# Optimization experiments

Hardware: AMD Instinct MI355X
Metric: run time of the kernel (lower is better)

## Reference

```python
import jax, jax.numpy as jnp
import numpy as np

DIM = 1024
NUM_HEADS = 16
BATCH = 4
SEQ = 2048
SCALE = (DIM // NUM_HEADS) ** -0.5
MASK_VAL = -10000000.0


def setup_inputs() -> dict:
    key = jax.random.key(0)
    k1, k2, k3, k4 = jax.random.split(key, 4)
    inputs = jax.random.normal(k1, (BATCH, SEQ, DIM), dtype=jnp.float32)
    # xavier-ish scaling for weights
    W_qkv = jax.random.normal(k2, (3 * DIM, DIM), dtype=jnp.float32) * (1.0 / np.sqrt(DIM))
    W_fc = jax.random.normal(k3, (DIM, DIM), dtype=jnp.float32) * (1.0 / np.sqrt(DIM))
    b_fc = jnp.zeros((DIM,), dtype=jnp.float32)
    padding_mask = jax.random.randint(k4, (BATCH, SEQ), 0, 2, dtype=jnp.int32)
    return {"inputs": inputs, "W_qkv": W_qkv, "W_fc": W_fc, "b_fc": b_fc,
            "padding_mask": padding_mask}


def reference(inputs, W_qkv, W_fc, b_fc, padding_mask):
    B, N, C = inputs.shape
    H = NUM_HEADS
    Dh = C // H
    # qkv projection (torch Linear: x @ W.T), [B,N,3C]
    qkv = jnp.einsum('bnc,oc->bno', inputs, W_qkv)
    qkv = qkv.reshape(B, N, 3, H, Dh).transpose(2, 0, 3, 1, 4)  # [3,B,H,N,Dh]
    q, k, v = qkv[0], qkv[1], qkv[2]
    att = jnp.einsum('bhqd,bhkd->bhqk', q, k) * SCALE  # [B,H,N,N]
    mask = padding_mask[:, None, None, :]              # [B,1,1,N]
    att = jnp.where(mask > 0, jnp.float32(MASK_VAL), att)
    att = jax.nn.softmax(att, axis=-1)
    x = jnp.einsum('bhqk,bhkd->bhqd', att, v)          # [B,H,N,Dh]
    x = x.transpose(0, 2, 1, 3).reshape(B, N, C)       # [B,N,C]
    out = jnp.einsum('bnc,oc->bno', x, W_fc) + b_fc
    return out
```

## Files before the change

kernel.cpp:

```cpp
#include <hip/hip_runtime.h>
#include <stdint.h>

constexpr int kDim  = 1024;
constexpr int kH    = 16;
constexpr int kB    = 4;
constexpr int kSeq  = 2048;
constexpr int kDh   = 64;
constexpr int kMTot = kB * kSeq;
constexpr int kNQkv = 3 * kDim;
constexpr float kScale = 0.125f;
constexpr float kLog2e = 1.44269504088896f;
constexpr float kC1    = kScale * kLog2e;
constexpr float kMaxSub = 10.0f;
constexpr float kMk2Un   = -kMaxSub * kLog2e;
constexpr float kMk2Mask = -1.0e9f;
constexpr int kPld = 72;
constexpr int kCld = 136;

typedef __attribute__((ext_vector_type(8))) short short8;
typedef __attribute__((ext_vector_type(4))) float floatx4;

__device__ __forceinline__ unsigned short f2bf(float f) {
  union { float f; unsigned u; } v; v.f = f;
  unsigned r = v.u + 0x7fffu + ((v.u >> 16) & 1u);
  return (unsigned short)(r >> 16);
}
__device__ __forceinline__ unsigned short f2bf_fast(float f) {
  union { float f; unsigned u; } v; v.f = f;
  return (unsigned short)((v.u + 0x8000u) >> 16);
}
__device__ __forceinline__ float vexp2(float x) {
  float r; asm("v_exp_f32 %0, %1" : "=v"(r) : "v"(x)); return r;
}
__device__ __forceinline__ void gl2lds16(const void* g, void* l) {
  __builtin_amdgcn_global_load_lds(
      (const __attribute__((address_space(1))) unsigned int*)g,
      (__attribute__((address_space(3))) unsigned int*)l, 16, 0, 0);
}

__global__ void __launch_bounds__(256) cvt_scan(
    const float4* __restrict__ x, const float4* __restrict__ wq,
    const float4* __restrict__ wf,
    ushort4* __restrict__ xb, ushort4* __restrict__ wqb, ushort4* __restrict__ wfb,
    const int* __restrict__ pm, int* __restrict__ cidx, int* __restrict__ nkd) {
  const int X4  = (kMTot * kDim) / 4;
  const int WQ4 = (kNQkv * kDim) / 4;
  const int NCVT = 12288;
  if (blockIdx.x >= NCVT) {
    const int b = blockIdx.x - NCVT;
    const int t = threadIdx.x;
    const int lane = t & 63, wv = t >> 6;
    __shared__ int wsum[4];
    __shared__ int woff[5];
    int base = t * 8;
    int keep[8]; int cnt = 0;
#pragma unroll
    for (int j = 0; j < 8; j++) {
      keep[j] = (pm[b * kSeq + base + j] <= 0) ? 1 : 0;
      cnt += keep[j];
    }
    int pre = cnt;
#pragma unroll
    for (int off = 1; off < 64; off <<= 1) {
      int v = __shfl_up(pre, off, 64);
      if (lane >= off) pre += v;
    }
    int excl = pre - cnt;
    if (lane == 63) wsum[wv] = pre;
    __syncthreads();
    if (t == 0) {
      int s = 0;
#pragma unroll
      for (int w = 0; w < 4; w++) { woff[w] = s; s += wsum[w]; }
      woff[4] = s;
      nkd[b] = s;
    }
    __syncthreads();
    const int nk = woff[4];
    int kp = woff[wv] + excl;
#pragma unroll
    for (int j = 0; j < 8; j++) {
      int n = base + j;
      int pos = keep[j] ? kp : nk + (n - kp);
      cidx[b * kSeq + pos] = b * kSeq + n;
      kp += keep[j];
    }
    return;
  }
  int i = blockIdx.x * 256 + threadIdx.x;
  float4 v; ushort4* dst;
  if (i < X4)            { v = x[i];             dst = xb  + i; }
  else if (i < X4 + WQ4) { v = wq[i - X4];       dst = wqb + (i - X4); }
  else                   { v = wf[i - X4 - WQ4]; dst = wfb + (i - X4 - WQ4); }
  ushort4 o;
  o.x = f2bf(v.x); o.y = f2bf(v.y); o.z = f2bf(v.z); o.w = f2bf(v.w);
  *dst = o;
}

__global__ void __launch_bounds__(512, 2) gemm_qkv(
    const unsigned short* __restrict__ xb, const unsigned short* __restrict__ wqb,
    const int* __restrict__ cidx, const int* __restrict__ nkd,
    unsigned short* __restrict__ qb, unsigned short* __restrict__ kb,
    unsigned short* __restrict__ vtb) {
  const int tN = blockIdx.x * 256, tM = blockIdx.y * 256;
  const int which = tN >> 10;
  const int b = tM >> 11, tMloc = tM & 2047;
  if (which != 0) {
    if (tMloc >= nkd[b]) return;
  }
  extern __shared__ __attribute__((aligned(16))) unsigned short smem[];
  unsigned short* As0 = smem;
  unsigned short* Bs0 = smem + 16384;
  unsigned short* As1 = smem + 32768;
  unsigned short* Bs1 = smem + 49152;

  const int t = threadIdx.x;
  const int lane = t & 63, wv = t >> 6;
  const int wm = (wv >> 2) << 7;
  const int wn = (wv & 3) << 6;
  const int lrow = lane & 15, quad = lane >> 4, l7 = lane & 7;
  const int srow = t >> 3;
  const int pu8 = (t & 7) * 8;
  const int lu8 = ((t & 7) ^ (srow & 7)) * 8;
  const int off0 = (quad ^ l7) * 8;

  const unsigned short* arow[4];
#pragma unroll
  for (int p = 0; p < 4; p++) {
    int r = tM + srow + p * 64;
    int rid = (which == 0) ? r : cidx[r];
    arow[p] = xb + (int64_t)rid * kDim + lu8;
  }
  const unsigned short* brow = wqb + (int64_t)(tN + srow) * kDim + lu8;

  floatx4 acc[8][4];
  floatx4 zero = {0.f, 0.f, 0.f, 0.f};
#pragma unroll
  for (int mi = 0; mi < 8; mi++)
#pragma unroll
    for (int ni = 0; ni < 4; ni++) acc[mi][ni] = zero;

#define STAGE_B(buf, p, k0) gl2lds16(brow + (int64_t)(p) * 64 * kDim + (k0), \
                                     (buf) + ((p) * 64 + srow) * 64 + pu8)
#define STAGE_A(buf, p, k0) gl2lds16(arow[p] + (k0), \
                                     (buf) + ((p) * 64 + srow) * 64 + pu8)
#define BARRIER() { asm volatile("" ::: "memory"); \
                    __builtin_amdgcn_s_barrier(); \
                    asm volatile("" ::: "memory"); }
#define LDA(q) { \
    const unsigned short* Ar0_ = Ac + (wm + (2*(q)) * 16 + lrow) * 64; \
    const unsigned short* Ar1_ = Ac + (wm + (2*(q)+1) * 16 + lrow) * 64; \
    af00 = *(const short8*)(Ar0_ + off0); \
    af01 = *(const short8*)(Ar0_ + (off0 ^ 32)); \
    af10 = *(const short8*)(Ar1_ + off0); \
    af11 = *(const short8*)(Ar1_ + (off0 ^ 32)); }
#define MFMAQ(q) { \
    __builtin_amdgcn_s_setprio(1); \
    _Pragma("unroll") \
    for (int ni = 0; ni < 4; ni++) { \
      acc[2*(q)][ni]   = __builtin_amdgcn_mfma_f32_16x16x32_bf16(af00, bfr[ni][0], acc[2*(q)][ni],   0, 0, 0); \
      acc[2*(q)+1][ni] = __builtin_amdgcn_mfma_f32_16x16x32_bf16(af10, bfr[ni][0], acc[2*(q)+1][ni], 0, 0, 0); \
    } \
    _Pragma("unroll") \
    for (int ni = 0; ni < 4; ni++) { \
      acc[2*(q)][ni]   = __builtin_amdgcn_mfma_f32_16x16x32_bf16(af01, bfr[ni][1], acc[2*(q)][ni],   0, 0, 0); \
      acc[2*(q)+1][ni] = __builtin_amdgcn_mfma_f32_16x16x32_bf16(af11, bfr[ni][1], acc[2*(q)+1][ni], 0, 0, 0); \
    } \
    __builtin_amdgcn_s_setprio(0); }

  STAGE_B(Bs0, 0, 0); STAGE_B(Bs0, 1, 0); STAGE_B(Bs0, 2, 0); STAGE_B(Bs0, 3, 0);
  STAGE_A(As0, 0, 0); STAGE_A(As0, 2, 0); STAGE_A(As0, 1, 0); STAGE_A(As0, 3, 0);
  asm volatile("s_waitcnt vmcnt(2)" ::: "memory");
  BARRIER();

  for (int tt = 0; tt < 16; ++tt) {
    unsigned short* Ac = (tt & 1) ? As1 : As0;
    unsigned short* Bc = (tt & 1) ? Bs1 : Bs0;
    unsigned short* An = (tt & 1) ? As0 : As1;
    unsigned short* Bn = (tt & 1) ? Bs0 : Bs1;
    const int kn = (tt + 1) * 64;
    const bool more = (tt < 15);

    short8 bfr[4][2];
    short8 af00, af01, af10, af11;

#pragma unroll
    for (int ni = 0; ni < 4; ni++) {
      const unsigned short* Br_ = Bc + (wn + ni * 16 + lrow) * 64;
      bfr[ni][0] = *(const short8*)(Br_ + off0);
      bfr[ni][1] = *(const short8*)(Br_ + (off0 ^ 32));
    }
    LDA(0);
    if (more) { STAGE_B(Bn, 0, kn); STAGE_B(Bn, 1, kn); }
    BARRIER();
    MFMAQ(0);
    BARRIER();
    LDA(1);
    if (more) { STAGE_B(Bn, 2, kn); STAGE_B(Bn, 3, kn); }
    BARRIER();
    MFMAQ(1);
    if (more) { asm volatile("s_waitcnt vmcnt(4)" ::: "memory"); }
    else      { asm volatile("s_waitcnt vmcnt(0)" ::: "memory"); }
    BARRIER();
    LDA(2);
    if (more) { STAGE_A(An, 0, kn); STAGE_A(An, 2, kn); }
    BARRIER();
    MFMAQ(2);
    BARRIER();
    LDA(3);
    if (more) { STAGE_A(An, 1, kn); STAGE_A(An, 3, kn); }
    BARRIER();
    MFMAQ(3);
    asm volatile("s_waitcnt vmcnt(2)" ::: "memory");
    BARRIER();
  }
#undef STAGE_B
#undef STAGE_A
#undef LDA
#undef MFMAQ

  unsigned short* Cs = smem;
  const bool vblk = (which == 2);
  const int h4 = (tN >> 6) & 15;
#pragma unroll
  for (int h = 0; h < 2; h++) {
    const bool writer = (((wv & 3) >> 1) == h);
    const int cwn = (wv & 1) * 64;
    if (!vblk) {
      if (writer) {
#pragma unroll
        for (int mi = 0; mi < 8; mi++)
#pragma unroll
          for (int ni = 0; ni < 4; ni++)
#pragma unroll
            for (int r = 0; r < 4; r++) {
              int row = wm + mi * 16 + quad * 4 + r;
              int c = cwn + ni * 16 + lrow;
              Cs[row * kCld + c] = f2bf(acc[mi][ni][r]);
            }
      }
      asm volatile("s_waitcnt lgkmcnt(0)" ::: "memory");
      BARRIER();
      unsigned short* qk = (which == 0) ? qb : kb;
#pragma unroll
      for (int g = 0; g < 2; g++) {
        int hh = (h4 + h * 2 + g) & 15;
        unsigned short* base = qk + ((int64_t)((b << 4) + hh) << 17)
                               + (int64_t)tMloc * 64;
#pragma unroll
        for (int it = 0; it < 4; it++) {
          int off = it * 4096 + t * 8;
          int n = off >> 6;
          int d = off & 63;
          *(short8*)(base + off) = *(const short8*)(Cs + n * kCld + g * 64 + d);
        }
      }
      BARRIER();
    } else {
      if (writer) {
#pragma unroll
        for (int mi = 0; mi < 8; mi++)
#pragma unroll
          for (int ni = 0; ni < 4; ni++)
#pragma unroll
            for (int r = 0; r < 4; r++) {
              int row = wm + mi * 16 + quad * 4 + r;
              int c = cwn + ni * 16 + lrow;
              Cs[c * 264 + row] = f2bf(acc[mi][ni][r]);
            }
      }
      asm volatile("s_waitcnt lgkmcnt(0)" ::: "memory");
      BARRIER();
#pragma unroll
      for (int g = 0; g < 2; g++) {
        int hh = (h4 + h * 2 + g) & 15;
        unsigned short* vbase = vtb + ((int64_t)((b << 4) + hh) << 17) + tMloc;
#pragma unroll
        for (int it = 0; it < 4; it++) {
          int off = it * 512 + t;
          int d = off >> 5, c8 = off & 31;
          *(short8*)(vbase + (int64_t)d * 2048 + c8 * 8) =
              *(const short8*)(Cs + (g * 64 + d) * 264 + c8 * 8);
        }
      }
      BARRIER();
    }
  }
#undef BARRIER
}

__global__ void __launch_bounds__(256, 4) attn(
    const unsigned short* __restrict__ qb, const unsigned short* __restrict__ kb,
    const unsigned short* __restrict__ vtb, const int* __restrict__ nkd,
    unsigned short* __restrict__ xab) {
  __shared__ __attribute__((aligned(16))) unsigned short Ks[64 * 64];
  __shared__ __attribute__((aligned(16))) unsigned short Vs[64 * 64];
  __shared__ __attribute__((aligned(16))) unsigned short Ps[4][2][16 * kPld];

  const int t = threadIdx.x, lane = t & 63, wv = t >> 6;
  const int lrow = lane & 15, quad = lane >> 4, l7 = lane & 7;
  const int qblk = blockIdx.x & 15, bh = blockIdx.x >> 4;
  const int b = bh >> 4, h = bh & 15;
  const int q0 = qblk * 128;
  const int srow = t >> 3;
  const int pu8 = (t & 7) * 8;
  const int lu8 = ((t & 7) ^ (srow & 7)) * 8;
  const int off0 = (quad ^ l7) * 8;

  const int nk  = nkd[b];
  const int nkt = (nk + 63) >> 6;

  const unsigned short* Qb0 = qb + ((int64_t)bh * kSeq + q0 + wv * 16 + lrow) * kDh;
  short8 qf[2][2];
  qf[0][0] = *(const short8*)(Qb0 + quad * 8);
  qf[0][1] = *(const short8*)(Qb0 + 32 + quad * 8);
  qf[1][0] = *(const short8*)(Qb0 + 64 * kDh + quad * 8);
  qf[1][1] = *(const short8*)(Qb0 + 64 * kDh + 32 + quad * 8);

  float l_run[2][4];
  floatx4 o_acc[2][4];
  floatx4 zero = {0.f, 0.f, 0.f, 0.f};
#pragma unroll
  for (int t2 = 0; t2 < 2; t2++) {
#pragma unroll
    for (int r = 0; r < 4; r++) l_run[t2][r] = 0.f;
#pragma unroll
    for (int di = 0; di < 4; di++) o_acc[t2][di] = zero;
  }

  const unsigned short* Kbase = kb  + (int64_t)bh * kSeq * kDh;
  const unsigned short* Vbase = vtb + (int64_t)bh * kDh * kSeq;

  for (int kt = 0; kt < nkt; ++kt) {
    const int k0 = kt * 64;
    {
      int r0 = srow, r1 = srow + 32;
      gl2lds16(Kbase + (int64_t)(k0 + r0) * kDh + lu8, Ks + r0 * 64 + pu8);
      gl2lds16(Kbase + (int64_t)(k0 + r1) * kDh + lu8, Ks + r1 * 64 + pu8);
      gl2lds16(Vbase + (int64_t)r0 * kSeq + k0 + lu8,  Vs + r0 * 64 + pu8);
      gl2lds16(Vbase + (int64_t)r1 * kSeq + k0 + lu8,  Vs + r1 * 64 + pu8);
    }
    __syncthreads();

    floatx4 s[2][4];
#pragma unroll
    for (int ni = 0; ni < 4; ni++) {
      const unsigned short* Kr = Ks + (ni * 16 + lrow) * 64;
      short8 kf0 = *(const short8*)(Kr + off0);
      short8 kf1 = *(const short8*)(Kr + (off0 ^ 32));
#pragma unroll
      for (int t2 = 0; t2 < 2; t2++) {
        floatx4 tmp = __builtin_amdgcn_mfma_f32_16x16x32_bf16(qf[t2][0], kf0, zero, 0, 0, 0);
        s[t2][ni]   = __builtin_amdgcn_mfma_f32_16x16x32_bf16(qf[t2][1], kf1, tmp, 0, 0, 0);
      }
    }
    float mk2[4];
#pragma unroll
    for (int c = 0; c < 4; c++)
      mk2[c] = (k0 + c * 16 + lrow < nk) ? kMk2Un : kMk2Mask;

#pragma unroll
    for (int t2 = 0; t2 < 2; t2++) {
      unsigned short* Pw = &Ps[wv][t2][0];
#pragma unroll
      for (int r = 0; r < 4; r++) {
        int prow = (quad * 4 + r) * kPld + lrow;
#pragma unroll
        for (int c = 0; c < 4; c++) {
          float p = vexp2(fmaf(s[t2][c][r], kC1, mk2[c]));
          l_run[t2][r] += p;
          Pw[prow + c * 16] = f2bf_fast(p);
        }
      }
    }
    asm volatile("s_waitcnt lgkmcnt(0)" ::: "memory");

#pragma unroll
    for (int ks = 0; ks < 2; ks++) {
      short8 pf0 = *(const short8*)(&Ps[wv][0][0] + lrow * kPld + ks * 32 + quad * 8);
      short8 pf1 = *(const short8*)(&Ps[wv][1][0] + lrow * kPld + ks * 32 + quad * 8);
      const int voff = off0 ^ (ks * 32);
#pragma unroll
      for (int di = 0; di < 4; di++) {
        short8 vf = *(const short8*)(Vs + (di * 16 + lrow) * 64 + voff);
        o_acc[0][di] = __builtin_amdgcn_mfma_f32_16x16x32_bf16(pf0, vf, o_acc[0][di], 0, 0, 0);
        o_acc[1][di] = __builtin_amdgcn_mfma_f32_16x16x32_bf16(pf1, vf, o_acc[1][di], 0, 0, 0);
      }
    }
    __syncthreads();
  }

#pragma unroll
  for (int t2 = 0; t2 < 2; t2++) {
#pragma unroll
    for (int r = 0; r < 4; r++) {
      float l = l_run[t2][r];
      l += __shfl_xor(l, 1, 64);
      l += __shfl_xor(l, 2, 64);
      l += __shfl_xor(l, 4, 64);
      l += __shfl_xor(l, 8, 64);
      float inv = 1.0f / l;
      int n = q0 + t2 * 64 + wv * 16 + quad * 4 + r;
      int64_t rowbase = ((int64_t)b * kSeq + n) * kDim + h * kDh;
#pragma unroll
      for (int di = 0; di < 4; di++)
        xab[rowbase + di * 16 + lrow] = f2bf(o_acc[t2][di][r] * inv);
    }
  }
}

__global__ void __launch_bounds__(256) gemm_fc(
    const unsigned short* __restrict__ xab, const unsigned short* __restrict__ wfb,
    const float* __restrict__ bfc, float* __restrict__ out) {
  __shared__ __attribute__((aligned(16))) unsigned short As[128 * 64];
  __shared__ __attribute__((aligned(16))) unsigned short Bs[64 * 64];
  const int tN = blockIdx.x * 64, tM = blockIdx.y * 128;
  const int t = threadIdx.x;
  const int lane = t & 63, wv = t >> 6;
  const int wm = (wv >> 1) << 6, wn = (wv & 1) << 5;
  const int lrow = lane & 15, quad = lane >> 4, l7 = lane & 7;
  const int srow = t >> 3;
  const int pu8 = (t & 7) * 8;
  const int lu8 = ((t & 7) ^ (srow & 7)) * 8;
  const int off0 = (quad ^ l7) * 8;

  floatx4 acc[4][2];
  floatx4 zero = {0.f, 0.f, 0.f, 0.f};
#pragma unroll
  for (int mi = 0; mi < 4; mi++)
#pragma unroll
    for (int ni = 0; ni < 2; ni++) acc[mi][ni] = zero;

  for (int k0 = 0; k0 < kDim; k0 += 64) {
#pragma unroll
    for (int p = 0; p < 4; ++p) {
      int r = srow + p * 32;
      gl2lds16(xab + (int64_t)(tM + r) * kDim + k0 + lu8, As + r * 64 + pu8);
    }
#pragma unroll
    for (int p = 0; p < 2; ++p) {
      int r = srow + p * 32;
      gl2lds16(wfb + (int64_t)(tN + r) * kDim + k0 + lu8, Bs + r * 64 + pu8);
    }
    __syncthreads();
#pragma unroll
    for (int kk = 0; kk < 64; kk += 32) {
      short8 af[4], bf[2];
#pragma unroll
      for (int mi = 0; mi < 4; mi++)
        af[mi] = *(const short8*)(As + (wm + mi * 16 + lrow) * 64 + (off0 ^ kk));
#pragma unroll
      for (int ni = 0; ni < 2; ni++)
        bf[ni] = *(const short8*)(Bs + (wn + ni * 16 + lrow) * 64 + (off0 ^ kk));
#pragma unroll
      for (int mi = 0; mi < 4; mi++)
#pragma unroll
        for (int ni = 0; ni < 2; ni++)
          acc[mi][ni] = __builtin_amdgcn_mfma_f32_16x16x32_bf16(af[mi], bf[ni], acc[mi][ni], 0, 0, 0);
    }
    __syncthreads();
  }

#pragma unroll
  for (int ni = 0; ni < 2; ni++) {
    int o = tN + wn + ni * 16 + lrow;
    float bias = bfc[o];
#pragma unroll
    for (int mi = 0; mi < 4; mi++) {
#pragma unroll
      for (int r = 0; r < 4; r++) {
        int i = tM + wm + mi * 16 + quad * 4 + r;
        out[(int64_t)i * kDim + o] = acc[mi][ni][r] + bias;
      }
    }
  }
}

extern "C" void kernel_launch(void* const* d_in, const int* in_sizes, int n_in,
                              void* d_out, int out_size, void* d_ws, size_t ws_size,
                              hipStream_t stream) {
  (void)in_sizes; (void)n_in; (void)out_size; (void)ws_size;
  const float* x    = (const float*)d_in[0];
  const float* wqkv = (const float*)d_in[1];
  const float* wfc  = (const float*)d_in[2];
  const float* bfc  = (const float*)d_in[3];
  const int*   pm   = (const int*)d_in[4];
  float* out = (float*)d_out;

  char* ws = (char*)d_ws;
  unsigned short* xb  = (unsigned short*)(ws);
  unsigned short* wqb = (unsigned short*)(ws + 16777216);
  unsigned short* wfb = (unsigned short*)(ws + 23068672);
  unsigned short* qb  = (unsigned short*)(ws + 25165824);
  unsigned short* kb  = (unsigned short*)(ws + 41943040);
  unsigned short* vtb = (unsigned short*)(ws + 58720256);
  int*            cidx= (int*)(ws + 75497472);
  int*            nkd = (int*)(ws + 75530240);
  unsigned short* xab = xb;

  static bool s_attr_set = false;
  if (!s_attr_set) {
    (void)hipFuncSetAttribute((const void*)gemm_qkv,
                              hipFuncAttributeMaxDynamicSharedMemorySize, 131072);
    s_attr_set = true;
  }

  cvt_scan<<<12288 + kB, 256, 0, stream>>>(
      (const float4*)x, (const float4*)wqkv, (const float4*)wfc,
      (ushort4*)xb, (ushort4*)wqb, (ushort4*)wfb, pm, cidx, nkd);
  gemm_qkv<<<dim3(kNQkv / 256, kMTot / 256), 512, 131072, stream>>>(
      xb, wqb, cidx, nkd, qb, kb, vtb);
  attn<<<kB * kH * (kSeq / 128), 256, 0, stream>>>(qb, kb, vtb, nkd, xab);
  gemm_fc<<<dim3(kDim / 64, kMTot / 128), 256, 0, stream>>>(xab, wfb, bfc, out);
}
```

Measured before the change: 236.7 us.

## Make QKV GEMM persistent with atomic tile scheduler and 128-row tail tiles

Converts the QKV projection GEMM from a 2D grid with early-exit blocks into a persistent kernel of 256 workgroups. Each workgroup claims tiles through a global atomic counter that cvt_scan resets, and the tile list is built from the compacted kept-key counts so no empty K/V tiles are launched. Partial tail tiles of 128 rows skip half the A staging and MFMA work. The goal is less launch waste and better load balance across CUs, at the cost of a global atomic and a block-wide sync per tile plus extra control flow inside the main loop.

Result: no change. 238.5 us (+0.8%).

```diff
diff --git a/kernel.cpp b/kernel.cpp
--- a/kernel.cpp
+++ b/kernel.cpp
@@ -42,7 +42,8 @@
     const float4* __restrict__ x, const float4* __restrict__ wq,
     const float4* __restrict__ wf,
     ushort4* __restrict__ xb, ushort4* __restrict__ wqb, ushort4* __restrict__ wfb,
-    const int* __restrict__ pm, int* __restrict__ cidx, int* __restrict__ nkd) {
+    const int* __restrict__ pm, int* __restrict__ cidx, int* __restrict__ nkd,
+    int* __restrict__ ctr) {
   const int X4  = (kMTot * kDim) / 4;
   const int WQ4 = (kNQkv * kDim) / 4;
   const int NCVT = 12288;
@@ -52,6 +53,7 @@
     const int lane = t & 63, wv = t >> 6;
     __shared__ int wsum[4];
     __shared__ int woff[5];
+    if (b == 0 && t == 0) *ctr = 256;
     int base = t * 8;
     int keep[8]; int cnt = 0;
 #pragma unroll
@@ -100,15 +102,11 @@
 __global__ void __launch_bounds__(512, 2) gemm_qkv(
     const unsigned short* __restrict__ xb, const unsigned short* __restrict__ wqb,
     const int* __restrict__ cidx, const int* __restrict__ nkd,
+    int* __restrict__ ctr,
     unsigned short* __restrict__ qb, unsigned short* __restrict__ kb,
     unsigned short* __restrict__ vtb) {
-  const int tN = blockIdx.x * 256, tM = blockIdx.y * 256;
-  const int which = tN >> 10;
-  const int b = tM >> 11, tMloc = tM & 2047;
-  if (which != 0) {
-    if (tMloc >= nkd[b]) return;
-  }
   extern __shared__ __attribute__((aligned(16))) unsigned short smem[];
+  __shared__ int s_slot;
   unsigned short* As0 = smem;
   unsigned short* Bs0 = smem + 16384;
   unsigned short* As1 = smem + 32768;
@@ -124,21 +122,12 @@
   const int lu8 = ((t & 7) ^ (srow & 7)) * 8;
   const int off0 = (quad ^ l7) * 8;
 
-  const unsigned short* arow[4];
-#pragma unroll
-  for (int p = 0; p < 4; p++) {
-    int r = tM + srow + p * 64;
-    int rid = (which == 0) ? r : cidx[r];
-    arow[p] = xb + (int64_t)rid * kDim + lu8;
-  }
-  const unsigned short* brow = wqb + (int64_t)(tN + srow) * kDim + lu8;
-
-  floatx4 acc[8][4];
-  floatx4 zero = {0.f, 0.f, 0.f, 0.f};
-#pragma unroll
-  for (int mi = 0; mi < 8; mi++)
-#pragma unroll
-    for (int ni = 0; ni < 4; ni++) acc[mi][ni] = zero;
+  const int rr0 = (nkd[0] + 127) >> 7, rr1 = (nkd[1] + 127) >> 7;
+  const int rr2 = (nkd[2] + 127) >> 7, rr3 = (nkd[3] + 127) >> 7;
+  const int tb0 = (rr0 + 1) >> 1, tb1 = (rr1 + 1) >> 1;
+  const int tb2 = (rr2 + 1) >> 1, tb3 = (rr3 + 1) >> 1;
+  const int pA = tb0, pB = pA + tb1, pC = pB + tb2, pD = pC + tb3;
+  const int NT = 128 + 8 * pD;
 
 #define STAGE_B(buf, p, k0) gl2lds16(brow + (int64_t)(p) * 64 * kDim + (k0), \
                                      (buf) + ((p) * 64 + srow) * 64 + pu8)
@@ -168,124 +157,191 @@
     } \
     __builtin_amdgcn_s_setprio(0); }
 
-  STAGE_B(Bs0, 0, 0); STAGE_B(Bs0, 1, 0); STAGE_B(Bs0, 2, 0); STAGE_B(Bs0, 3, 0);
-  STAGE_A(As0, 0, 0); STAGE_A(As0, 2, 0); STAGE_A(As0, 1, 0); STAGE_A(As0, 3, 0);
-  asm volatile("s_waitcnt vmcnt(2)" ::: "memory");
-  BARRIER();
-
-  for (int tt = 0; tt < 16; ++tt) {
-    unsigned short* Ac = (tt & 1) ? As1 : As0;
-    unsigned short* Bc = (tt & 1) ? Bs1 : Bs0;
-    unsigned short* An = (tt & 1) ? As0 : As1;
-    unsigned short* Bn = (tt & 1) ? Bs0 : Bs1;
-    const int kn = (tt + 1) * 64;
-    const bool more = (tt < 15);
-
-    short8 bfr[4][2];
-    short8 af00, af01, af10, af11;
-
-#pragma unroll
-    for (int ni = 0; ni < 4; ni++) {
-      const unsigned short* Br_ = Bc + (wn + ni * 16 + lrow) * 64;
-      bfr[ni][0] = *(const short8*)(Br_ + off0);
-      bfr[ni][1] = *(const short8*)(Br_ + (off0 ^ 32));
-    }
-    LDA(0);
-    if (more) { STAGE_B(Bn, 0, kn); STAGE_B(Bn, 1, kn); }
+  int slot = blockIdx.x;
+  while (slot < NT) {
+    int which, tN, tMl, bb, rbv;
+    if (slot < 128) {
+      which = 0; tN = (slot & 3) * 256;
+      int tMg = (slot >> 2) * 256;
+      bb = tMg >> 11; tMl = tMg & 2047; rbv = 16;
+    } else {
+      int id = slot - 128;
+      const int TK = 4 * pD;
+      which = (id < TK) ? 1 : 2;
+      if (which == 2) id -= TK;
+      int col = id & 3, j = id >> 2;
+      int pj;
+      if (j < pA)      { bb = 0; pj = j;      rbv = rr0; }
+      else if (j < pB) { bb = 1; pj = j - pA; rbv = rr1; }
+      else if (j < pC) { bb = 2; pj = j - pB; rbv = rr2; }
+      else             { bb = 3; pj = j - pC; rbv = rr3; }
+      tMl = pj * 256;
+      tN = (which == 1 ? 1024 : 2048) + col * 256;
+    }
+    int nrows;
+    if (which == 0) nrows = 256;
+    else { int rem = rbv * 128 - tMl; nrows = (rem >= 256) ? 256 : 128; }
+    const bool na4 = (nrows == 256);
+    const bool act = (wm < nrows);
+    const bool vblk = (which == 2);
+
+    const unsigned short* arow[4];
+#pragma unroll
+    for (int p = 0; p < 4; p++) {
+      int pe = (!na4 && p > 1) ? 1 : p;
+      int rl = tMl + pe * 64 + srow;
+      int rid = (which == 0) ? (bb * 2048 + rl) : cidx[bb * 2048 + rl];
+      arow[p] = xb + (int64_t)rid * kDim + lu8;
+    }
+    const unsigned short* brow = wqb + (int64_t)(tN + srow) * kDim + lu8;
+
+    floatx4 acc[8][4];
+    floatx4 zero = {0.f, 0.f, 0.f, 0.f};
+#pragma unroll
+    for (int mi = 0; mi < 8; mi++)
+#pragma unroll
+      for (int ni = 0; ni < 4; ni++) acc[mi][ni] = zero;
+
+    STAGE_B(Bs0, 0, 0); STAGE_B(Bs0, 1, 0); STAGE_B(Bs0, 2, 0); STAGE_B(Bs0, 3, 0);
+    STAGE_A(As0, 0, 0);
+    if (na4) {
+      STAGE_A(As0, 2, 0); STAGE_A(As0, 1, 0); STAGE_A(As0, 3, 0);
+      asm volatile("s_waitcnt vmcnt(2)" ::: "memory");
+    } else {
+      STAGE_A(As0, 1, 0);
+      asm volatile("s_waitcnt vmcnt(1)" ::: "memory");
+    }
     BARRIER();
-    MFMAQ(0);
-    BARRIER();
-    LDA(1);
-    if (more) { STAGE_B(Bn, 2, kn); STAGE_B(Bn, 3, kn); }
-    BARRIER();
-    MFMAQ(1);
-    if (more) { asm volatile("s_waitcnt vmcnt(4)" ::: "memory"); }
-    else      { asm volatile("s_waitcnt vmcnt(0)" ::: "memory"); }
-    BARRIER();
-    LDA(2);
-    if (more) { STAGE_A(An, 0, kn); STAGE_A(An, 2, kn); }
-    BARRIER();
-    MFMAQ(2);
-    BARRIER();
-    LDA(3);
-    if (more) { STAGE_A(An, 1, kn); STAGE_A(An, 3, kn); }
-    BARRIER();
-    MFMAQ(3);
-    asm volatile("s_waitcnt vmcnt(2)" ::: "memory");
-    BARRIER();
+
+    for (int tt = 0; tt < 16; ++tt) {
+      unsigned short* Ac = (tt & 1) ? As1 : As0;
+      unsigned short* Bc = (tt & 1) ? Bs1 : Bs0;
+      unsigned short* An = (tt & 1) ? As0 : As1;
+      unsigned short* Bn = (tt & 1) ? Bs0 : Bs1;
+      const int kn = (tt + 1) * 64;
+      const bool more = (tt < 15);
+
+      short8 bfr[4][2];
+      short8 af00, af01, af10, af11;
+
+      if (act) {
+#pragma unroll
+        for (int ni = 0; ni < 4; ni++) {
+          const unsigned short* Br_ = Bc + (wn + ni * 16 + lrow) * 64;
+          bfr[ni][0] = *(const short8*)(Br_ + off0);
+          bfr[ni][1] = *(const short8*)(Br_ + (off0 ^ 32));
+        }
+        LDA(0);
+      }
+      if (more) { STAGE_B(Bn, 0, kn); STAGE_B(Bn, 1, kn); }
+      BARRIER();
+      if (act) MFMAQ(0);
+      BARRIER();
+      if (act) LDA(1);
+      if (more) { STAGE_B(Bn, 2, kn); STAGE_B(Bn, 3, kn); }
+      BARRIER();
+      if (act) MFMAQ(1);
+      if (more) { asm volatile("s_waitcnt vmcnt(4)" ::: "memory"); }
+      else      { asm volatile("s_waitcnt vmcnt(0)" ::: "memory"); }
+      BARRIER();
+      if (act) LDA(2);
+      if (more) {
+        STAGE_A(An, 0, kn);
+        if (na4) { STAGE_A(An, 2, kn); STAGE_A(An, 1, kn); STAGE_A(An, 3, kn); }
+        else     { STAGE_A(An, 1, kn); }
+      }
+      BARRIER();
+      if (act) MFMAQ(2);
+      BARRIER();
+      if (act) LDA(3);
+      BARRIER();
+      if (act) MFMAQ(3);
+      if (more) {
+        if (na4) { asm volatile("s_waitcnt vmcnt(2)" ::: "memory"); }
+        else     { asm volatile("s_waitcnt vmcnt(1)" ::: "memory"); }
+      } else {
+        asm volatile("s_waitcnt vmcnt(0)" ::: "memory");
+      }
+      BARRIER();
+    }
+
+    unsigned short* Cs = smem;
+    const int h4 = (tN >> 6) & 15;
+#pragma unroll
+    for (int h = 0; h < 2; h++) {
+      const bool writer = ((((wv & 3) >> 1) == h) && act);
+      const int cwn = (wv & 1) * 64;
+      if (!vblk) {
+        if (writer) {
+#pragma unroll
+          for (int mi = 0; mi < 8; mi++)
+#pragma unroll
+            for (int ni = 0; ni < 4; ni++)
+#pragma unroll
+              for (int r = 0; r < 4; r++) {
+                int row = wm + mi * 16 + quad * 4 + r;
+                int c = cwn + ni * 16 + lrow;
+                Cs[row * kCld + c] = f2bf(acc[mi][ni][r]);
+              }
+        }
+        asm volatile("s_waitcnt lgkmcnt(0)" ::: "memory");
+        BARRIER();
+        unsigned short* qk = (which == 0) ? qb : kb;
+        const int itn = nrows >> 6;
+#pragma unroll
+        for (int g = 0; g < 2; g++) {
+          int hh = (h4 + h * 2 + g) & 15;
+          unsigned short* base = qk + ((int64_t)((bb << 4) + hh) << 17)
+                                 + (int64_t)tMl * 64;
+          for (int it = 0; it < itn; it++) {
+            int off = it * 4096 + t * 8;
+            int n = off >> 6;
+            int d = off & 63;
+            *(short8*)(base + off) = *(const short8*)(Cs + n * kCld + g * 64 + d);
+          }
+        }
+        BARRIER();
+      } else {
+        if (writer) {
+#pragma unroll
+          for (int mi = 0; mi < 8; mi++)
+#pragma unroll
+            for (int ni = 0; ni < 4; ni++)
+#pragma unroll
+              for (int r = 0; r < 4; r++) {
+                int row = wm + mi * 16 + quad * 4 + r;
+                int c = cwn + ni * 16 + lrow;
+                Cs[c * 264 + row] = f2bf(acc[mi][ni][r]);
+              }
+        }
+        asm volatile("s_waitcnt lgkmcnt(0)" ::: "memory");
+        BARRIER();
+        const int c8n = nrows >> 3;
+#pragma unroll
+        for (int g = 0; g < 2; g++) {
+          int hh = (h4 + h * 2 + g) & 15;
+          unsigned short* vbase = vtb + (((int64_t)((bb << 4) + hh)) << 17) + tMl;
+#pragma unroll
+          for (int it = 0; it < 4; it++) {
+            int off = it * 512 + t;
+            int d = off >> 5, c8 = off & 31;
+            if (c8 < c8n)
+              *(short8*)(vbase + (int64_t)d * 2048 + c8 * 8) =
+                  *(const short8*)(Cs + (g * 64 + d) * 264 + c8 * 8);
+          }
+        }
+        BARRIER();
+      }
+    }
+
+    if (t == 0) s_slot = atomicAdd(ctr, 1);
+    __syncthreads();
+    slot = s_slot;
   }
 #undef STAGE_B
 #undef STAGE_A
 #undef LDA
 #undef MFMAQ
-
-  unsigned short* Cs = smem;
-  const bool vblk = (which == 2);
-  const int h4 = (tN >> 6) & 15;
-#pragma unroll
-  for (int h = 0; h < 2; h++) {
-    const bool writer = (((wv & 3) >> 1) == h);
-    const int cwn = (wv & 1) * 64;
-    if (!vblk) {
-      if (writer) {
-#pragma unroll
-        for (int mi = 0; mi < 8; mi++)
-#pragma unroll
-          for (int ni = 0; ni < 4; ni++)
-#pragma unroll
-            for (int r = 0; r < 4; r++) {
-              int row = wm + mi * 16 + quad * 4 + r;
-              int c = cwn + ni * 16 + lrow;
-              Cs[row * kCld + c] = f2bf(acc[mi][ni][r]);
-            }
-      }
-      asm volatile("s_waitcnt lgkmcnt(0)" ::: "memory");
-      BARRIER();
-      unsigned short* qk = (which == 0) ? qb : kb;
-#pragma unroll
-      for (int g = 0; g < 2; g++) {
-        int hh = (h4 + h * 2 + g) & 15;
-        unsigned short* base = qk + ((int64_t)((b << 4) + hh) << 17)
-                               + (int64_t)tMloc * 64;
-#pragma unroll
-        for (int it = 0; it < 4; it++) {
-          int off = it * 4096 + t * 8;
-          int n = off >> 6;
-          int d = off & 63;
-          *(short8*)(base + off) = *(const short8*)(Cs + n * kCld + g * 64 + d);
-        }
-      }
-      BARRIER();
-    } else {
-      if (writer) {
-#pragma unroll
-        for (int mi = 0; mi < 8; mi++)
-#pragma unroll
-          for (int ni = 0; ni < 4; ni++)
-#pragma unroll
-            for (int r = 0; r < 4; r++) {
-              int row = wm + mi * 16 + quad * 4 + r;
-              int c = cwn + ni * 16 + lrow;
-              Cs[c * 264 + row] = f2bf(acc[mi][ni][r]);
-            }
-      }
-      asm volatile("s_waitcnt lgkmcnt(0)" ::: "memory");
-      BARRIER();
-#pragma unroll
-      for (int g = 0; g < 2; g++) {
-        int hh = (h4 + h * 2 + g) & 15;
-        unsigned short* vbase = vtb + ((int64_t)((b << 4) + hh) << 17) + tMloc;
-#pragma unroll
-        for (int it = 0; it < 4; it++) {
-          int off = it * 512 + t;
-          int d = off >> 5, c8 = off & 31;
-          *(short8*)(vbase + (int64_t)d * 2048 + c8 * 8) =
-              *(const short8*)(Cs + (g * 64 + d) * 264 + c8 * 8);
-        }
-      }
-      BARRIER();
-    }
-  }
 #undef BARRIER
 }
 
@@ -496,6 +552,7 @@
   unsigned short* vtb = (unsigned short*)(ws + 58720256);
   int*            cidx= (int*)(ws + 75497472);
   int*            nkd = (int*)(ws + 75530240);
+  int*            ctr = (int*)(ws + 75530256);
   unsigned short* xab = xb;
 
   static bool s_attr_set = false;
@@ -507,9 +564,9 @@
 
   cvt_scan<<<12288 + kB, 256, 0, stream>>>(
       (const float4*)x, (const float4*)wqkv, (const float4*)wfc,
-      (ushort4*)xb, (ushort4*)wqb, (ushort4*)wfb, pm, cidx, nkd);
-  gemm_qkv<<<dim3(kNQkv / 256, kMTot / 256), 512, 131072, stream>>>(
-      xb, wqb, cidx, nkd, qb, kb, vtb);
+      (ushort4*)xb, (ushort4*)wqb, (ushort4*)wfb, pm, cidx, nkd, ctr);
+  gemm_qkv<<<256, 512, 131072, stream>>>(
+      xb, wqb, cidx, nkd, ctr, qb, kb, vtb);
   attn<<<kB * kH * (kSeq / 128), 256, 0, stream>>>(qb, kb, vtb, nkd, xab);
   gemm_fc<<<dim3(kDim / 64, kMTot / 128), 256, 0, stream>>>(xab, wfb, bfc, out);
 }
```
